# Kernel optimization log

Measured on AMD Instinct MI355X. Metric: run time of the kernel, lower is better.

Reference implementation:

```python
import jax, jax.numpy as jnp
import numpy as np

EMBED_DIM = 64
NUM_HEADS = 8
D_K = EMBED_DIM // NUM_HEADS  # 8
B, S = 8, 1024


def setup_inputs() -> dict:
    key = jax.random.key(0)
    ks = jax.random.split(key, 10)
    f32 = jnp.float32
    lim = 1.0 / np.sqrt(EMBED_DIM)
    def lin(k):
        kw, kb = jax.random.split(k)
        w = jax.random.uniform(kw, (EMBED_DIM, EMBED_DIM), f32, -lim, lim)
        b = jax.random.uniform(kb, (EMBED_DIM,), f32, -lim, lim)
        return w, b
    wq, bq = lin(ks[0])
    wk, bk = lin(ks[1])
    wv, bv = lin(ks[2])
    wo, bo = lin(ks[3])
    theta = jax.random.normal(ks[4], (EMBED_DIM,), f32)  # trainable RY angles, one per wire
    x = jax.random.normal(ks[5], (B, S, EMBED_DIM), f32)
    return {"x": x, "wq": wq, "bq": bq, "wk": wk, "bk": bk,
            "wv": wv, "bv": bv, "theta": theta, "wo": wo, "bo": bo}


def _quantum_map(t, theta):
    # Per-qubit circuit on |0>: RX(t_i) encode, RY(theta_i), <PauliZ_i>.
    # Product state => <Z_i> = cos(theta_i) * cos(t_i) exactly.
    return jnp.cos(theta) * jnp.cos(t.reshape(-1, EMBED_DIM))  # [N, E]


def reference(x, wq, bq, wk, bk, wv, bv, theta, wo, bo):
    # Linear QKV (torch nn.Linear: x @ W^T + b)
    q = x @ wq.T + bq
    k = x @ wk.T + bk
    v = x @ wv.T + bv
    # Quantum measurement map, flattened over batch*seq (as in the original)
    q_q = _quantum_map(q, theta)  # [N, E], N = B*S
    k_q = _quantum_map(k, theta)
    v_q = _quantum_map(v, theta)
    # Full flattened attention: [N, N] scores (original never reshapes back)
    scores = (q_q @ k_q.T) / jnp.sqrt(jnp.asarray(D_K, x.dtype))
    attn = jax.nn.softmax(scores, axis=-1)  # dropout is identity in eval
    out = attn @ v_q  # [N, E]
    return out @ wo.T + bo
```

## Files before the change

### kernel.cpp

```cpp
#include <hip/hip_runtime.h>
#include <hip/hip_bf16.h>

#define NQ 8192
#define DIM 64
#define SPLITS 16
#define QBLK 128
#define WQ 64
#define BN 64
#define KEYS_PER_SPLIT (NQ / SPLITS)
#define NTILES (KEYS_PER_SPLIT / BN)
#define GRID_FLASH ((NQ / QBLK) * SPLITS)
#define MERGEB 1024
#define MROWS (NQ / MERGEB)
#define SC2 0.51012301920911057f
#define KSTR 72

typedef short s8v __attribute__((ext_vector_type(8)));
typedef short s4v __attribute__((ext_vector_type(4)));
typedef float f4v __attribute__((ext_vector_type(4)));
typedef int   i4v __attribute__((ext_vector_type(4)));

__device__ __forceinline__ float b2f(short s) {
  unsigned int u = ((unsigned int)(unsigned short)s) << 16;
  return __uint_as_float(u);
}
__device__ __forceinline__ float b2f_lo(unsigned int u) {
  return __uint_as_float(u << 16);
}
__device__ __forceinline__ float b2f_hi(unsigned int u) {
  return __uint_as_float(u & 0xffff0000u);
}
__device__ __forceinline__ short f2b(float f) {
  __hip_bfloat16 h = __float2bfloat16(f);
  return *reinterpret_cast<short*>(&h);
}
__device__ __forceinline__ int pack_bf16x2(float a, float b) {
  union { __hip_bfloat162 h; int i; } u;
  u.h = __float22bfloat162_rn(make_float2(a, b));
  return u.i;
}
__device__ __forceinline__ float fast_exp2(float x) {
#if __has_builtin(__builtin_amdgcn_exp2f)
  return __builtin_amdgcn_exp2f(x);
#else
  return exp2f(x);
#endif
}

__global__ __launch_bounds__(64) void qkv_kernel(
    const float* __restrict__ x,
    const float* __restrict__ wq, const float* __restrict__ bq,
    const float* __restrict__ wk, const float* __restrict__ bk,
    const float* __restrict__ wv, const float* __restrict__ bv,
    const float* __restrict__ theta,
    short* __restrict__ qq, short* __restrict__ kvT) {
  int lane = threadIdx.x & 63;
  int l15 = lane & 15, quad = lane >> 4;
  int tg = blockIdx.x;
  int mg = blockIdx.y;
  int n = tg * 16 + l15;

  const float* W  = (mg == 0) ? wq : (mg == 1) ? wk : wv;
  const float* Bb = (mg == 0) ? bq : (mg == 1) ? bk : bv;

  const float* xr = x + (size_t)n * DIM + quad * 8;
  float4 x0 = *(const float4*)&xr[0];
  float4 x1 = *(const float4*)&xr[4];
  float4 x2 = *(const float4*)&xr[32];
  float4 x3 = *(const float4*)&xr[36];
  s8v xf0 = {f2b(x0.x), f2b(x0.y), f2b(x0.z), f2b(x0.w),
             f2b(x1.x), f2b(x1.y), f2b(x1.z), f2b(x1.w)};
  s8v xf1 = {f2b(x2.x), f2b(x2.y), f2b(x2.z), f2b(x2.w),
             f2b(x3.x), f2b(x3.y), f2b(x3.z), f2b(x3.w)};

  size_t tb = (size_t)(n >> 6) * 8192;
  int nperm = (n & 3) | ((n & 16) >> 2);
  size_t vbase = tb + 4096 + ((n & 32) >> 5) * 2048 + ((n & 15) >> 2) * 128 + nperm;

#pragma unroll
  for (int i = 0; i < 4; ++i) {
    const float* wr = W + (size_t)(i * 16 + l15) * DIM + quad * 8;
    float4 a0 = *(const float4*)&wr[0];
    float4 a1 = *(const float4*)&wr[4];
    float4 a2 = *(const float4*)&wr[32];
    float4 a3 = *(const float4*)&wr[36];
    s8v wf0 = {f2b(a0.x), f2b(a0.y), f2b(a0.z), f2b(a0.w),
               f2b(a1.x), f2b(a1.y), f2b(a1.z), f2b(a1.w)};
    s8v wf1 = {f2b(a2.x), f2b(a2.y), f2b(a2.z), f2b(a2.w),
               f2b(a3.x), f2b(a3.y), f2b(a3.z), f2b(a3.w)};
    f4v acc = (f4v){0.f, 0.f, 0.f, 0.f};
    acc = __builtin_amdgcn_mfma_f32_16x16x32_bf16(wf0, xf0, acc, 0, 0, 0);
    acc = __builtin_amdgcn_mfma_f32_16x16x32_bf16(wf1, xf1, acc, 0, 0, 0);
    int d0 = i * 16 + quad * 4;
    float4 bias = *(const float4*)&Bb[d0];
    float4 th4 = *(const float4*)&theta[d0];
    float y0 = __cosf(acc[0] + bias.x) * __cosf(th4.x);
    float y1 = __cosf(acc[1] + bias.y) * __cosf(th4.y);
    float y2 = __cosf(acc[2] + bias.z) * __cosf(th4.z);
    float y3 = __cosf(acc[3] + bias.w) * __cosf(th4.w);
    if (mg == 0) {
      s4v p = {f2b(SC2 * y0), f2b(SC2 * y1), f2b(SC2 * y2), f2b(SC2 * y3)};
      *(s4v*)&qq[(size_t)n * DIM + d0] = p;
    } else if (mg == 1) {
      int e = d0;
      size_t idx = tb + ((n & 63) >> 4) * 1024 + (e >> 5) * 512 +
                   ((e & 31) >> 3) * 128 + (n & 15) * 8 + (e & 7);
      s4v p = {f2b(y0), f2b(y1), f2b(y2), f2b(y3)};
      *(s4v*)&kvT[idx] = p;
    } else {
      float ys[4] = {y0, y1, y2, y3};
#pragma unroll
      for (int r = 0; r < 4; ++r) {
        int e = d0 + r;
        kvT[vbase + (e >> 4) * 512 + (e & 15) * 8] = f2b(ys[r]);
      }
    }
  }
}

#if __has_builtin(__builtin_amdgcn_global_load_lds)
#define DMA_CHUNK(srcp, dstp) \
  __builtin_amdgcn_global_load_lds( \
      (const __attribute__((address_space(1))) void*)(srcp), \
      (__attribute__((address_space(3))) void*)(dstp), 16, 0, 0)
#else
#define DMA_CHUNK(srcp, dstp) \
  { *(s8v*)((short*)(dstp) + (threadIdx.x & 63) * 8) = \
        *(const s8v*)((const short*)(srcp)); }
#endif

__global__ __launch_bounds__(128, 2) void flash_kernel(
    const short* __restrict__ qq, const short* __restrict__ kvT,
    short* __restrict__ pO, short* __restrict__ pL) {
  __shared__ __align__(16) short lds[2][8192];

  int tid = threadIdx.x;
  int wave = tid >> 6, lane = tid & 63;
  int l15 = lane & 15, quad = lane >> 4;
  int qblock = blockIdx.x >> 4, split = blockIdx.x & 15;
  int qbase = qblock * QBLK + wave * WQ;

  s8v qf[4][2];
#pragma unroll
  for (int qt = 0; qt < 4; ++qt) {
    const short* qr = qq + (qbase + qt * 16 + l15) * DIM + quad * 8;
    qf[qt][0] = *(const s8v*)qr;
    qf[qt][1] = *(const s8v*)(qr + 32);
  }

  const short ONE = (short)0x3F80;
  const s8v ones = {ONE, ONE, ONE, ONE, ONE, ONE, ONE, ONE};

  f4v o[4][4], ol[4];
#pragma unroll
  for (int qt = 0; qt < 4; ++qt) {
    ol[qt] = (f4v){0.f, 0.f, 0.f, 0.f};
#pragma unroll
    for (int c = 0; c < 4; ++c) o[qt][c] = (f4v){0.f, 0.f, 0.f, 0.f};
  }

  int gt0 = split * NTILES;

#define STAGE(T, BUF)                                                        \
  {                                                                          \
    const short* s_ = kvT + (size_t)(gt0 + (T)) * 8192 + wave * 4096 +       \
                      lane * 8;                                              \
    short* d_ = &lds[BUF][wave * 4096];                                      \
    _Pragma("unroll") for (int c2 = 0; c2 < 8; ++c2)                         \
        DMA_CHUNK(s_ + c2 * 512, d_ + c2 * 512);                             \
  }

  STAGE(0, 0)

  for (int t = 0; t < NTILES; ++t) {
    __syncthreads();
    if (t + 1 < NTILES) STAGE(t + 1, (t + 1) & 1)

    const short* kb = lds[t & 1];
    const short* vb = lds[t & 1] + 4096;

#pragma unroll
    for (int kp = 0; kp < 2; ++kp) {
      i4v pai[4];
#pragma unroll
      for (int h = 0; h < 2; ++h) {
        int kt = kp * 2 + h;
        s8v kf0 = *(const s8v*)&kb[(kt * 2) * 512 + lane * 8];
        s8v kf1 = *(const s8v*)&kb[(kt * 2 + 1) * 512 + lane * 8];
#pragma unroll
        for (int qt = 0; qt < 4; ++qt) {
          f4v acc = (f4v){0.f, 0.f, 0.f, 0.f};
          acc = __builtin_amdgcn_mfma_f32_16x16x32_bf16(kf0, qf[qt][0], acc, 0, 0, 0);
          acc = __builtin_amdgcn_mfma_f32_16x16x32_bf16(kf1, qf[qt][1], acc, 0, 0, 0);
          pai[qt][h * 2]     = pack_bf16x2(fast_exp2(acc[0]), fast_exp2(acc[1]));
          pai[qt][h * 2 + 1] = pack_bf16x2(fast_exp2(acc[2]), fast_exp2(acc[3]));
        }
      }
      __builtin_amdgcn_s_setprio(1);
#pragma unroll
      for (int qt = 0; qt < 4; ++qt)
        ol[qt] = __builtin_amdgcn_mfma_f32_16x16x32_bf16(
            __builtin_bit_cast(s8v, pai[qt]), ones, ol[qt], 0, 0, 0);
#pragma unroll
      for (int c = 0; c < 4; ++c) {
        s8v vf = *(const s8v*)&vb[(kp * 4 + c) * 512 + lane * 8];
#pragma unroll
        for (int qt = 0; qt < 4; ++qt)
          o[qt][c] = __builtin_amdgcn_mfma_f32_16x16x32_bf16(
              __builtin_bit_cast(s8v, pai[qt]), vf, o[qt][c], 0, 0, 0);
      }
      __builtin_amdgcn_s_setprio(0);
    }
  }

#pragma unroll
  for (int qt = 0; qt < 4; ++qt) {
#pragma unroll
    for (int r = 0; r < 4; ++r) {
      int q = qbase + qt * 16 + quad * 4 + r;
      short* dst = pO + ((size_t)split * NQ + q) * DIM;
#pragma unroll
      for (int c = 0; c < 4; ++c) dst[c * 16 + l15] = f2b(o[qt][c][r]);
      if (l15 == 0) pL[(size_t)split * NQ + q] = f2b(ol[qt][r]);
    }
  }
}

__global__ __launch_bounds__(256) void merge_kernel(
    const short* __restrict__ pO, const short* __restrict__ pL,
    const float* __restrict__ wo, const float* __restrict__ bo,
    float* __restrict__ out) {
  __shared__ __align__(16) short wsh[DIM * KSTR];
  __shared__ __align__(16) float att[MROWS * DIM];
  int tid = threadIdx.x;
  int q0 = blockIdx.x * MROWS;
  for (int i = tid; i < DIM * 16; i += 256) {
    int r = i >> 4, c4 = (i & 15) << 2;
    float4 w = *(const float4*)&wo[r * DIM + c4];
    s4v p = {f2b(w.x), f2b(w.y), f2b(w.z), f2b(w.w)};
    *(s4v*)&wsh[r * KSTR + c4] = p;
  }
  {
    int e2 = (tid & 31) * 2, rg8 = tid >> 5;
    int q = q0 + rg8;
    const short* psrc = pO + (size_t)q * DIM + e2;
    const short* lsrc = pL + q;
    float a0 = 0.f, a1 = 0.f, l = 0.f;
#pragma unroll
    for (int sp = 0; sp < SPLITS; ++sp) {
      unsigned int u = *(const unsigned int*)&psrc[(size_t)sp * NQ * DIM];
      a0 += b2f_lo(u);
      a1 += b2f_hi(u);
      l += b2f(lsrc[(size_t)sp * NQ]);
    }
#if __has_builtin(__builtin_amdgcn_rcpf)
    float ri = __builtin_amdgcn_rcpf(l);
#else
    float ri = 1.f / l;
#endif
    att[rg8 * DIM + e2] = a0 * ri;
    att[rg8 * DIM + e2 + 1] = a1 * ri;
  }
  __syncthreads();
  int e = tid & 63, rg = tid >> 6;
  for (int rr = rg; rr < MROWS; rr += 4) {
    float acc = bo[e];
#pragma unroll
    for (int c8 = 0; c8 < 8; ++c8) {
      s8v w = *(const s8v*)&wsh[e * KSTR + c8 * 8];
      const float* ar = &att[rr * DIM + c8 * 8];
      acc += ar[0] * b2f(w[0]) + ar[1] * b2f(w[1]) + ar[2] * b2f(w[2]) + ar[3] * b2f(w[3])
           + ar[4] * b2f(w[4]) + ar[5] * b2f(w[5]) + ar[6] * b2f(w[6]) + ar[7] * b2f(w[7]);
    }
    out[(size_t)(q0 + rr) * DIM + e] = acc;
  }
}

extern "C" void kernel_launch(void* const* d_in, const int* in_sizes, int n_in,
                              void* d_out, int out_size, void* d_ws, size_t ws_size,
                              hipStream_t stream) {
  const float* x  = (const float*)d_in[0];
  const float* wq = (const float*)d_in[1];
  const float* bq = (const float*)d_in[2];
  const float* wk = (const float*)d_in[3];
  const float* bk = (const float*)d_in[4];
  const float* wv = (const float*)d_in[5];
  const float* bv = (const float*)d_in[6];
  const float* th = (const float*)d_in[7];
  const float* wo = (const float*)d_in[8];
  const float* bo = (const float*)d_in[9];

  char* ws = (char*)d_ws;
  short* qq  = (short*)(ws);
  short* kvT = (short*)(ws + (1u << 20));
  short* pO  = (short*)(ws + (3u << 20));
  short* pL  = (short*)(ws + (19u << 20));

  hipLaunchKernelGGL(qkv_kernel, dim3(NQ / 16, 3), dim3(64), 0, stream,
                     x, wq, bq, wk, bk, wv, bv, th, qq, kvT);
  hipLaunchKernelGGL(flash_kernel, dim3(GRID_FLASH), dim3(128), 0, stream,
                     qq, kvT, pO, pL);
  hipLaunchKernelGGL(merge_kernel, dim3(MERGEB), dim3(256), 0, stream,
                     pO, pL, wo, bo, (float*)d_out);
}
```

Baseline: 114.7 us.

## Use single-wave flash blocks with 32-key double-buffered DMA and no barriers

Each flash block shrinks from two waves covering 128 queries to one wave covering 64 queries, which doubles the grid. Keys are staged in 32-key steps through a smaller double-buffered LDS area. Because each block is a single wave, __syncthreads is replaced by explicit vmcnt waits on the async global-to-LDS loads. This removes the block-wide barrier and shrinks LDS use, so more blocks can be resident. In exchange, K/V tiles are reloaded twice as often across blocks, and correctness now depends on the hand-written waitcnt ordering.

```diff
diff --git a/kernel.cpp b/kernel.cpp
--- a/kernel.cpp
+++ b/kernel.cpp
@@ -4,12 +4,10 @@
 #define NQ 8192
 #define DIM 64
 #define SPLITS 16
-#define QBLK 128
-#define WQ 64
-#define BN 64
+#define FQB 64
 #define KEYS_PER_SPLIT (NQ / SPLITS)
-#define NTILES (KEYS_PER_SPLIT / BN)
-#define GRID_FLASH ((NQ / QBLK) * SPLITS)
+#define NSTEPS (KEYS_PER_SPLIT / 32)
+#define GRID_FLASH ((NQ / FQB) * SPLITS)
 #define MERGEB 1024
 #define MROWS (NQ / MERGEB)
 #define SC2 0.51012301920911057f
@@ -129,16 +127,15 @@
         *(const s8v*)((const short*)(srcp)); }
 #endif
 
-__global__ __launch_bounds__(128, 2) void flash_kernel(
+__global__ __launch_bounds__(64, 2) void flash_kernel(
     const short* __restrict__ qq, const short* __restrict__ kvT,
     short* __restrict__ pO, short* __restrict__ pL) {
-  __shared__ __align__(16) short lds[2][8192];
-
-  int tid = threadIdx.x;
-  int wave = tid >> 6, lane = tid & 63;
+  __shared__ __align__(16) short lds[2][4096];
+
+  int lane = threadIdx.x & 63;
   int l15 = lane & 15, quad = lane >> 4;
   int qblock = blockIdx.x >> 4, split = blockIdx.x & 15;
-  int qbase = qblock * QBLK + wave * WQ;
+  int qbase = qblock * FQB;
 
   s8v qf[4][2];
 #pragma unroll
@@ -147,6 +144,7 @@
     qf[qt][0] = *(const s8v*)qr;
     qf[qt][1] = *(const s8v*)(qr + 32);
   }
+  asm volatile("s_waitcnt vmcnt(0)" ::: "memory");
 
   const short ONE = (short)0x3F80;
   const s8v ones = {ONE, ONE, ONE, ONE, ONE, ONE, ONE, ONE};
@@ -159,58 +157,60 @@
     for (int c = 0; c < 4; ++c) o[qt][c] = (f4v){0.f, 0.f, 0.f, 0.f};
   }
 
-  int gt0 = split * NTILES;
-
-#define STAGE(T, BUF)                                                        \
+  const short* kvs = kvT + (size_t)(split * (KEYS_PER_SPLIT / 64)) * 8192 +
+                     lane * 8;
+#define STAGE32(S, BUF)                                                      \
   {                                                                          \
-    const short* s_ = kvT + (size_t)(gt0 + (T)) * 8192 + wave * 4096 +       \
-                      lane * 8;                                              \
-    short* d_ = &lds[BUF][wave * 4096];                                      \
-    _Pragma("unroll") for (int c2 = 0; c2 < 8; ++c2)                         \
-        DMA_CHUNK(s_ + c2 * 512, d_ + c2 * 512);                             \
-  }
-
-  STAGE(0, 0)
-
-  for (int t = 0; t < NTILES; ++t) {
-    __syncthreads();
-    if (t + 1 < NTILES) STAGE(t + 1, (t + 1) & 1)
-
-    const short* kb = lds[t & 1];
-    const short* vb = lds[t & 1] + 4096;
-
-#pragma unroll
-    for (int kp = 0; kp < 2; ++kp) {
-      i4v pai[4];
-#pragma unroll
-      for (int h = 0; h < 2; ++h) {
-        int kt = kp * 2 + h;
-        s8v kf0 = *(const s8v*)&kb[(kt * 2) * 512 + lane * 8];
-        s8v kf1 = *(const s8v*)&kb[(kt * 2 + 1) * 512 + lane * 8];
-#pragma unroll
-        for (int qt = 0; qt < 4; ++qt) {
-          f4v acc = (f4v){0.f, 0.f, 0.f, 0.f};
-          acc = __builtin_amdgcn_mfma_f32_16x16x32_bf16(kf0, qf[qt][0], acc, 0, 0, 0);
-          acc = __builtin_amdgcn_mfma_f32_16x16x32_bf16(kf1, qf[qt][1], acc, 0, 0, 0);
-          pai[qt][h * 2]     = pack_bf16x2(fast_exp2(acc[0]), fast_exp2(acc[1]));
-          pai[qt][h * 2 + 1] = pack_bf16x2(fast_exp2(acc[2]), fast_exp2(acc[3]));
-        }
+    const short* s_ = kvs + ((S) >> 1) * 8192 + ((S) & 1) * 2048;            \
+    short* d_ = &lds[BUF][0];                                                \
+    _Pragma("unroll") for (int c2 = 0; c2 < 4; ++c2) {                       \
+      DMA_CHUNK(s_ + c2 * 512, d_ + c2 * 512);                               \
+      DMA_CHUNK(s_ + 4096 + c2 * 512, d_ + 2048 + c2 * 512);                 \
+    }                                                                        \
+  }
+
+  STAGE32(0, 0)
+
+  for (int s = 0; s < NSTEPS; ++s) {
+    if (s + 1 < NSTEPS) {
+      STAGE32(s + 1, (s + 1) & 1)
+      asm volatile("s_waitcnt vmcnt(8)" ::: "memory");
+    } else {
+      asm volatile("s_waitcnt vmcnt(0)" ::: "memory");
+    }
+    __builtin_amdgcn_sched_barrier(0);
+
+    const short* kb = lds[s & 1];
+    const short* vb = kb + 2048;
+
+    i4v pai[4];
+#pragma unroll
+    for (int h = 0; h < 2; ++h) {
+      s8v kf0 = *(const s8v*)&kb[(h * 2) * 512 + lane * 8];
+      s8v kf1 = *(const s8v*)&kb[(h * 2 + 1) * 512 + lane * 8];
+#pragma unroll
+      for (int qt = 0; qt < 4; ++qt) {
+        f4v acc = (f4v){0.f, 0.f, 0.f, 0.f};
+        acc = __builtin_amdgcn_mfma_f32_16x16x32_bf16(kf0, qf[qt][0], acc, 0, 0, 0);
+        acc = __builtin_amdgcn_mfma_f32_16x16x32_bf16(kf1, qf[qt][1], acc, 0, 0, 0);
+        pai[qt][h * 2]     = pack_bf16x2(fast_exp2(acc[0]), fast_exp2(acc[1]));
+        pai[qt][h * 2 + 1] = pack_bf16x2(fast_exp2(acc[2]), fast_exp2(acc[3]));
       }
-      __builtin_amdgcn_s_setprio(1);
+    }
+    __builtin_amdgcn_s_setprio(1);
+#pragma unroll
+    for (int qt = 0; qt < 4; ++qt)
+      ol[qt] = __builtin_amdgcn_mfma_f32_16x16x32_bf16(
+          __builtin_bit_cast(s8v, pai[qt]), ones, ol[qt], 0, 0, 0);
+#pragma unroll
+    for (int c = 0; c < 4; ++c) {
+      s8v vf = *(const s8v*)&vb[c * 512 + lane * 8];
 #pragma unroll
       for (int qt = 0; qt < 4; ++qt)
-        ol[qt] = __builtin_amdgcn_mfma_f32_16x16x32_bf16(
-            __builtin_bit_cast(s8v, pai[qt]), ones, ol[qt], 0, 0, 0);
-#pragma unroll
-      for (int c = 0; c < 4; ++c) {
-        s8v vf = *(const s8v*)&vb[(kp * 4 + c) * 512 + lane * 8];
-#pragma unroll
-        for (int qt = 0; qt < 4; ++qt)
-          o[qt][c] = __builtin_amdgcn_mfma_f32_16x16x32_bf16(
-              __builtin_bit_cast(s8v, pai[qt]), vf, o[qt][c], 0, 0, 0);
-      }
-      __builtin_amdgcn_s_setprio(0);
-    }
+        o[qt][c] = __builtin_amdgcn_mfma_f32_16x16x32_bf16(
+            __builtin_bit_cast(s8v, pai[qt]), vf, o[qt][c], 0, 0, 0);
+    }
+    __builtin_amdgcn_s_setprio(0);
   }
 
 #pragma unroll
@@ -298,7 +298,7 @@
 
   hipLaunchKernelGGL(qkv_kernel, dim3(NQ / 16, 3), dim3(64), 0, stream,
                      x, wq, bq, wk, bk, wv, bv, th, qq, kvT);
-  hipLaunchKernelGGL(flash_kernel, dim3(GRID_FLASH), dim3(128), 0, stream,
+  hipLaunchKernelGGL(flash_kernel, dim3(GRID_FLASH), dim3(FQB), 0, stream,
                      qq, kvT, pO, pL);
   hipLaunchKernelGGL(merge_kernel, dim3(MERGEB), dim3(256), 0, stream,
                      pO, pL, wo, bo, (float*)d_out);
```

Measured after the change: 113.6 us (median of 2 runs). Within noise of the previous version (-1.0%).
